# Kernel optimization log

Hardware: AMD Instinct MI355X
Metric: run time of the kernel (lower is better)

## Reference

```python
import jax, jax.numpy as jnp
import numpy as np

T = 16           # number of stochastic-computing cycles (sequential forward calls)
N = 2097152      # parallel stochastic lanes (flattened element count)
BUF_DEP = 4      # shift-register depth (default buf_dep)


def setup_inputs() -> dict:
    key = jax.random.key(0)
    k1, k2 = jax.random.split(key)
    # bitstreams: values in {0,1}, stored as float32 per bstype=torch.float
    dividend = jax.random.randint(k1, (T, N), 0, 2).astype(jnp.float32)
    divisor = jax.random.randint(k2, (T, N), 0, 2).astype(jnp.float32)
    # ShiftReg_init: sr[i] = i % 2, broadcast to input shape -> [BUF_DEP, N]
    sr_init = jnp.tile((jnp.arange(BUF_DEP) % 2).astype(jnp.float32)[:, None], (1, N))
    # 2-bit (log2(buf_dep)) 1-D Sobol sequence scaled to integers 0..3
    rng_table = jnp.array([0, 2, 3, 1], dtype=jnp.int32)
    return {"dividend": dividend, "divisor": divisor, "sr_init": sr_init, "rng_table": rng_table}


def reference(dividend, divisor, sr_init, rng_table):
    T_ = dividend.shape[0]
    buf_dep = sr_init.shape[0]
    # idx starts at 0 and increments each cycle; gather index = rng[idx % buf_dep]
    rng_idx = rng_table[jnp.arange(T_) % buf_dep]  # [T]

    def step(sr, xs):
        dvd, dvs, r = xs
        sel = (dvs == 1).astype(dvd.dtype)                     # divisor_eq_1
        hq = jax.lax.dynamic_index_in_dim(sr, r, axis=0, keepdims=False)  # historic_q [N]
        q = sel * dvd + (1 - sel) * hq                          # quotient [N]
        # ShiftReg push: new value at slot 0, others shift down, oldest dropped
        sr = jnp.concatenate([q[None], sr[:-1]], axis=0)
        return sr, q

    _, quotients = jax.lax.scan(step, sr_init, (dividend, divisor, rng_idx))
    return quotients  # [T, N]
```

## Files before the change

kernel.cpp:

```cpp
#include <hip/hip_runtime.h>


#define SC_T   16
#define SC_BUF 4
#define PHASE  8

typedef float v4f __attribute__((ext_vector_type(4)));

__global__ __launch_bounds__(256) void cordiv_kernel(
    const v4f* __restrict__ dividend,
    const v4f* __restrict__ divisor,
    const v4f* __restrict__ sr_init,
    const int* __restrict__ rng_table,
    v4f*       __restrict__ out,
    int n4)
{
    const int gid = blockIdx.x * blockDim.x + threadIdx.x;
    if (gid >= n4) return;

    const int r0 = rng_table[0];
    const int r1 = rng_table[1];
    const int r2 = rng_table[2];
    const int r3 = rng_table[3];
    const int rtab[SC_BUF] = {r0, r1, r2, r3};

    v4f sr0 = sr_init[0 * n4 + gid];
    v4f sr1 = sr_init[1 * n4 + gid];
    v4f sr2 = sr_init[2 * n4 + gid];
    v4f sr3 = sr_init[3 * n4 + gid];

    v4f dvd[PHASE], dvs[PHASE];

#pragma unroll
    for (int p = 0; p < SC_T / PHASE; ++p) {
        const int tbase = p * PHASE;

#pragma unroll
        for (int i = 0; i < PHASE; ++i) {
            dvd[i] = dividend[(tbase + i) * n4 + gid];
            dvs[i] = divisor [(tbase + i) * n4 + gid];
        }

#pragma unroll
        for (int i = 0; i < PHASE; ++i) {
            const int t = tbase + i;
            const int r = rtab[t & (SC_BUF - 1)];

            const v4f hq = (r == 0) ? sr0 : (r == 1) ? sr1
                         : (r == 2) ? sr2 : sr3;

            v4f q;
            q.x = (dvs[i].x == 1.0f) ? dvd[i].x : hq.x;
            q.y = (dvs[i].y == 1.0f) ? dvd[i].y : hq.y;
            q.z = (dvs[i].z == 1.0f) ? dvd[i].z : hq.z;
            q.w = (dvs[i].w == 1.0f) ? dvd[i].w : hq.w;

            __builtin_nontemporal_store(q, &out[t * n4 + gid]);

            sr3 = sr2; sr2 = sr1; sr1 = sr0; sr0 = q;
        }
    }
}

extern "C" void kernel_launch(void* const* d_in, const int* in_sizes, int n_in,
                              void* d_out, int out_size, void* d_ws, size_t ws_size,
                              hipStream_t stream) {
    const float* dividend = (const float*)d_in[0];
    const float* divisor  = (const float*)d_in[1];
    const float* sr_init  = (const float*)d_in[2];
    const int*   rng      = (const int*)d_in[3];
    float*       out      = (float*)d_out;

    const int n  = in_sizes[0] / SC_T;
    const int n4 = n / 4;

    const int block = 256;
    const int grid  = (n4 + block - 1) / block;

    cordiv_kernel<<<grid, block, 0, stream>>>(
        (const v4f*)dividend, (const v4f*)divisor,
        (const v4f*)sr_init, rng, (v4f*)out, n4);
}
```

Measured before the change: 373.9 us.

## Stage inputs through LDS with direct global-to-LDS loads in chunks of four

Input loads now use global_load_lds, which writes dividend and divisor straight into shared memory in chunks of four time steps instead of holding eight steps in registers. This cuts register pressure, and the intent is better occupancy on a bandwidth-bound stream. The bounds check is gone, so the kernel assumes n4 is a multiple of the block size. Stores switch from nontemporal to regular, and each chunk waits on vmcnt(0), which serialises loads against compute within a chunk.

```diff
diff --git a/kernel.cpp b/kernel.cpp
--- a/kernel.cpp
+++ b/kernel.cpp
@@ -1,13 +1,17 @@
 #include <hip/hip_runtime.h>
+#include <stdint.h>
 
 
 #define SC_T   16
 #define SC_BUF 4
-#define PHASE  8
+#define CHUNK  4
+#define BLOCK  256
 
 typedef float v4f __attribute__((ext_vector_type(4)));
+typedef const __attribute__((address_space(1))) void glb_void;
+typedef __attribute__((address_space(3))) void lds_void;
 
-__global__ __launch_bounds__(256) void cordiv_kernel(
+__global__ __launch_bounds__(BLOCK) void cordiv_kernel(
     const v4f* __restrict__ dividend,
     const v4f* __restrict__ divisor,
     const v4f* __restrict__ sr_init,
@@ -15,8 +19,12 @@
     v4f*       __restrict__ out,
     int n4)
 {
-    const int gid = blockIdx.x * blockDim.x + threadIdx.x;
-    if (gid >= n4) return;
+    __shared__ v4f lds_dvd[CHUNK][BLOCK];
+    __shared__ v4f lds_dvs[CHUNK][BLOCK];
+
+    const int tid   = threadIdx.x;
+    const int gid   = blockIdx.x * BLOCK + tid;
+    const int wbase = tid & ~63;
 
     const int r0 = rng_table[0];
     const int r1 = rng_table[1];
@@ -29,33 +37,39 @@
     v4f sr2 = sr_init[2 * n4 + gid];
     v4f sr3 = sr_init[3 * n4 + gid];
 
-    v4f dvd[PHASE], dvs[PHASE];
+#pragma unroll
+    for (int c = 0; c < SC_T / CHUNK; ++c) {
+#pragma unroll
+        for (int i = 0; i < CHUNK; ++i) {
+            const int t = c * CHUNK + i;
+            __builtin_amdgcn_global_load_lds(
+                (glb_void*)(dividend + (size_t)t * n4 + gid),
+                (lds_void*)&lds_dvd[i][wbase], 16, 0, 0);
+            __builtin_amdgcn_global_load_lds(
+                (glb_void*)(divisor + (size_t)t * n4 + gid),
+                (lds_void*)&lds_dvs[i][wbase], 16, 0, 0);
+        }
+
+        asm volatile("s_waitcnt vmcnt(0)" ::: "memory");
 
 #pragma unroll
-    for (int p = 0; p < SC_T / PHASE; ++p) {
-        const int tbase = p * PHASE;
+        for (int i = 0; i < CHUNK; ++i) {
+            const int t = c * CHUNK + i;
+            const int r = rtab[t & (SC_BUF - 1)];
 
-#pragma unroll
-        for (int i = 0; i < PHASE; ++i) {
-            dvd[i] = dividend[(tbase + i) * n4 + gid];
-            dvs[i] = divisor [(tbase + i) * n4 + gid];
-        }
-
-#pragma unroll
-        for (int i = 0; i < PHASE; ++i) {
-            const int t = tbase + i;
-            const int r = rtab[t & (SC_BUF - 1)];
+            const v4f dvd = lds_dvd[i][tid];
+            const v4f dvs = lds_dvs[i][tid];
 
             const v4f hq = (r == 0) ? sr0 : (r == 1) ? sr1
                          : (r == 2) ? sr2 : sr3;
 
             v4f q;
-            q.x = (dvs[i].x == 1.0f) ? dvd[i].x : hq.x;
-            q.y = (dvs[i].y == 1.0f) ? dvd[i].y : hq.y;
-            q.z = (dvs[i].z == 1.0f) ? dvd[i].z : hq.z;
-            q.w = (dvs[i].w == 1.0f) ? dvd[i].w : hq.w;
+            q.x = (dvs.x == 1.0f) ? dvd.x : hq.x;
+            q.y = (dvs.y == 1.0f) ? dvd.y : hq.y;
+            q.z = (dvs.z == 1.0f) ? dvd.z : hq.z;
+            q.w = (dvs.w == 1.0f) ? dvd.w : hq.w;
 
-            __builtin_nontemporal_store(q, &out[t * n4 + gid]);
+            out[(size_t)t * n4 + gid] = q;
 
             sr3 = sr2; sr2 = sr1; sr1 = sr0; sr0 = q;
         }
@@ -74,10 +88,9 @@
     const int n  = in_sizes[0] / SC_T;
     const int n4 = n / 4;
 
-    const int block = 256;
-    const int grid  = (n4 + block - 1) / block;
+    const int grid = (n4 + BLOCK - 1) / BLOCK;
 
-    cordiv_kernel<<<grid, block, 0, stream>>>(
+    cordiv_kernel<<<grid, BLOCK, 0, stream>>>(
         (const v4f*)dividend, (const v4f*)divisor,
         (const v4f*)sr_init, rng, (v4f*)out, n4);
 }
```

New measurement: 338.9 us. -9.4%, faster.

## Software-pipeline loads with inline asm and two lanes per thread

Applied to the files above, without the earlier changes.

Each thread now handles two vec4 lanes and streams the 16 time steps through a 3-slot register ring. Loads are issued two steps ahead via inline-asm global_load_dwordx4, and the code waits on explicit vmcnt counts, replacing the two batched 8-step load phases. Nontemporal stores become plain stores, and the bounds check is dropped because the grid assumes n4 divides by 512. The aim is steadier memory-level parallelism at lower register cost, but the hand-written vmcnt accounting is fragile and may fight the compiler's own waitcnt insertion.

```diff
diff --git a/kernel.cpp b/kernel.cpp
--- a/kernel.cpp
+++ b/kernel.cpp
@@ -1,11 +1,24 @@
 #include <hip/hip_runtime.h>
+#include <stdint.h>
 
 
-#define SC_T   16
-#define SC_BUF 4
-#define PHASE  8
+#define SC_T    16
+#define D_AHEAD 2
 
 typedef float v4f __attribute__((ext_vector_type(4)));
+
+__device__ __forceinline__ v4f gload(const v4f* __restrict__ p) {
+    v4f r;
+    asm volatile("global_load_dwordx4 %0, %1, off" : "=v"(r) : "v"(p));
+    return r;
+}
+
+#define PIN_WAIT(N, a, b, c, d)                                          \
+    asm volatile("s_waitcnt vmcnt(%c4)"                                  \
+                 : "+v"(a), "+v"(b), "+v"(c), "+v"(d) : "i"(N) : "memory")
+
+#define WAITN(t) (2 * ((t) >= 1) + 2 * ((t) >= 2) + \
+                  4 * ((t) + 1 < SC_T) + 4 * ((t) + 2 < SC_T))
 
 __global__ __launch_bounds__(256) void cordiv_kernel(
     const v4f* __restrict__ dividend,
@@ -15,51 +28,67 @@
     v4f*       __restrict__ out,
     int n4)
 {
-    const int gid = blockIdx.x * blockDim.x + threadIdx.x;
-    if (gid >= n4) return;
+    const int tid = threadIdx.x;
+    const int g0  = blockIdx.x * 512 + tid;
+    const int g1  = g0 + 256;
 
     const int r0 = rng_table[0];
     const int r1 = rng_table[1];
     const int r2 = rng_table[2];
     const int r3 = rng_table[3];
-    const int rtab[SC_BUF] = {r0, r1, r2, r3};
+    const int rtab[4] = {r0, r1, r2, r3};
 
-    v4f sr0 = sr_init[0 * n4 + gid];
-    v4f sr1 = sr_init[1 * n4 + gid];
-    v4f sr2 = sr_init[2 * n4 + gid];
-    v4f sr3 = sr_init[3 * n4 + gid];
+    v4f srA0 = sr_init[0 * n4 + g0], srA1 = sr_init[1 * n4 + g0],
+        srA2 = sr_init[2 * n4 + g0], srA3 = sr_init[3 * n4 + g0];
+    v4f srB0 = sr_init[0 * n4 + g1], srB1 = sr_init[1 * n4 + g1],
+        srB2 = sr_init[2 * n4 + g1], srB3 = sr_init[3 * n4 + g1];
+    asm volatile("" : "+v"(srA0), "+v"(srA1), "+v"(srA2), "+v"(srA3),
+                      "+v"(srB0), "+v"(srB1), "+v"(srB2), "+v"(srB3));
 
-    v4f dvd[PHASE], dvs[PHASE];
+    v4f bD[3][2], bS[3][2];
 
-#pragma unroll
-    for (int p = 0; p < SC_T / PHASE; ++p) {
-        const int tbase = p * PHASE;
+#define ISSUE(t) do {                                                     \
+        const int s_ = (t) % 3;                                           \
+        bD[s_][0] = gload(dividend + (size_t)(t) * n4 + g0);              \
+        bD[s_][1] = gload(dividend + (size_t)(t) * n4 + g1);              \
+        bS[s_][0] = gload(divisor  + (size_t)(t) * n4 + g0);              \
+        bS[s_][1] = gload(divisor  + (size_t)(t) * n4 + g1);              \
+    } while (0)
 
-#pragma unroll
-        for (int i = 0; i < PHASE; ++i) {
-            dvd[i] = dividend[(tbase + i) * n4 + gid];
-            dvs[i] = divisor [(tbase + i) * n4 + gid];
-        }
+#define STEP(t) do {                                                      \
+        if ((t) + D_AHEAD < SC_T) ISSUE((t) + D_AHEAD);                   \
+        const int s_ = (t) % 3;                                           \
+        PIN_WAIT(WAITN(t), bD[s_][0], bD[s_][1], bS[s_][0], bS[s_][1]);   \
+        const int r_ = rtab[(t) & 3];                                     \
+        const v4f hqA = (r_ == 0) ? srA0 : (r_ == 1) ? srA1               \
+                      : (r_ == 2) ? srA2 : srA3;                          \
+        const v4f hqB = (r_ == 0) ? srB0 : (r_ == 1) ? srB1               \
+                      : (r_ == 2) ? srB2 : srB3;                          \
+        v4f qA, qB;                                                       \
+        qA.x = (bS[s_][0].x == 1.0f) ? bD[s_][0].x : hqA.x;               \
+        qA.y = (bS[s_][0].y == 1.0f) ? bD[s_][0].y : hqA.y;               \
+        qA.z = (bS[s_][0].z == 1.0f) ? bD[s_][0].z : hqA.z;               \
+        qA.w = (bS[s_][0].w == 1.0f) ? bD[s_][0].w : hqA.w;               \
+        qB.x = (bS[s_][1].x == 1.0f) ? bD[s_][1].x : hqB.x;               \
+        qB.y = (bS[s_][1].y == 1.0f) ? bD[s_][1].y : hqB.y;               \
+        qB.z = (bS[s_][1].z == 1.0f) ? bD[s_][1].z : hqB.z;               \
+        qB.w = (bS[s_][1].w == 1.0f) ? bD[s_][1].w : hqB.w;               \
+        out[(size_t)(t) * n4 + g0] = qA;                                  \
+        out[(size_t)(t) * n4 + g1] = qB;                                  \
+        srA3 = srA2; srA2 = srA1; srA1 = srA0; srA0 = qA;                 \
+        srB3 = srB2; srB2 = srB1; srB1 = srB0; srB0 = qB;                 \
+    } while (0)
 
-#pragma unroll
-        for (int i = 0; i < PHASE; ++i) {
-            const int t = tbase + i;
-            const int r = rtab[t & (SC_BUF - 1)];
+    ISSUE(0);
+    ISSUE(1);
 
-            const v4f hq = (r == 0) ? sr0 : (r == 1) ? sr1
-                         : (r == 2) ? sr2 : sr3;
+    STEP(0);  STEP(1);  STEP(2);  STEP(3);
+    STEP(4);  STEP(5);  STEP(6);  STEP(7);
+    STEP(8);  STEP(9);  STEP(10); STEP(11);
+    STEP(12); STEP(13); STEP(14); STEP(15);
 
-            v4f q;
-            q.x = (dvs[i].x == 1.0f) ? dvd[i].x : hq.x;
-            q.y = (dvs[i].y == 1.0f) ? dvd[i].y : hq.y;
-            q.z = (dvs[i].z == 1.0f) ? dvd[i].z : hq.z;
-            q.w = (dvs[i].w == 1.0f) ? dvd[i].w : hq.w;
-
-            __builtin_nontemporal_store(q, &out[t * n4 + gid]);
-
-            sr3 = sr2; sr2 = sr1; sr1 = sr0; sr0 = q;
-        }
-    }
+#undef STEP
+#undef ISSUE
 }
 
 extern "C" void kernel_launch(void* const* d_in, const int* in_sizes, int n_in,
@@ -75,7 +104,7 @@
     const int n4 = n / 4;
 
     const int block = 256;
-    const int grid  = (n4 + block - 1) / block;
+    const int grid  = n4 / 512;
 
     cordiv_kernel<<<grid, block, 0, stream>>>(
         (const v4f*)dividend, (const v4f*)divisor,
```

After: 335.8 us. -10.2%, faster.

## Split cordiv into parallel select pass and sequential resolve pass

Applied to the files above, without the earlier changes.

Splits the single fused kernel into two launches. The first is a fully parallel pass over all T*N elements that writes the dividend where the divisor is 1 and a -1 sentinel elsewhere. The second walks the 16 cycles per lane, reading that intermediate back from the output buffer and filling sentinels from the shift register. The aim is more memory-level parallelism in the first pass, but it adds a full extra read and write of the output, drops the nontemporal stores, and adds a second launch. It also relies on grid sizes dividing evenly by 256.

```diff
diff --git a/kernel.cpp b/kernel.cpp
--- a/kernel.cpp
+++ b/kernel.cpp
@@ -1,64 +1,66 @@
 #include <hip/hip_runtime.h>
 
 
-#define SC_T   16
-#define SC_BUF 4
-#define PHASE  8
+#define SC_T 16
 
 typedef float v4f __attribute__((ext_vector_type(4)));
 
-__global__ __launch_bounds__(256) void cordiv_kernel(
-    const v4f* __restrict__ dividend,
-    const v4f* __restrict__ divisor,
+__global__ __launch_bounds__(256) void k_select(
+    const v4f* __restrict__ dvd,
+    const v4f* __restrict__ dvs,
+    v4f*       __restrict__ out,
+    int total4)
+{
+    const int i = blockIdx.x * 256 + threadIdx.x;
+    if (i >= total4) return;
+
+    const v4f a = dvd[i];
+    const v4f s = dvs[i];
+    v4f q;
+    q.x = (s.x == 1.0f) ? a.x : -1.0f;
+    q.y = (s.y == 1.0f) ? a.y : -1.0f;
+    q.z = (s.z == 1.0f) ? a.z : -1.0f;
+    q.w = (s.w == 1.0f) ? a.w : -1.0f;
+    out[i] = q;
+}
+
+__global__ __launch_bounds__(256) void k_resolve(
     const v4f* __restrict__ sr_init,
     const int* __restrict__ rng_table,
     v4f*       __restrict__ out,
     int n4)
 {
-    const int gid = blockIdx.x * blockDim.x + threadIdx.x;
-    if (gid >= n4) return;
+    const int g = blockIdx.x * 256 + threadIdx.x;
+    if (g >= n4) return;
 
     const int r0 = rng_table[0];
     const int r1 = rng_table[1];
     const int r2 = rng_table[2];
     const int r3 = rng_table[3];
-    const int rtab[SC_BUF] = {r0, r1, r2, r3};
+    const int rtab[4] = {r0, r1, r2, r3};
 
-    v4f sr0 = sr_init[0 * n4 + gid];
-    v4f sr1 = sr_init[1 * n4 + gid];
-    v4f sr2 = sr_init[2 * n4 + gid];
-    v4f sr3 = sr_init[3 * n4 + gid];
-
-    v4f dvd[PHASE], dvs[PHASE];
+    v4f sr0 = sr_init[0 * n4 + g];
+    v4f sr1 = sr_init[1 * n4 + g];
+    v4f sr2 = sr_init[2 * n4 + g];
+    v4f sr3 = sr_init[3 * n4 + g];
 
 #pragma unroll
-    for (int p = 0; p < SC_T / PHASE; ++p) {
-        const int tbase = p * PHASE;
+    for (int t = 0; t < SC_T; ++t) {
+        const int r = rtab[t & 3];
+        const v4f v = out[(size_t)t * n4 + g];
 
-#pragma unroll
-        for (int i = 0; i < PHASE; ++i) {
-            dvd[i] = dividend[(tbase + i) * n4 + gid];
-            dvs[i] = divisor [(tbase + i) * n4 + gid];
-        }
+        const v4f hq = (r == 0) ? sr0 : (r == 1) ? sr1
+                     : (r == 2) ? sr2 : sr3;
 
-#pragma unroll
-        for (int i = 0; i < PHASE; ++i) {
-            const int t = tbase + i;
-            const int r = rtab[t & (SC_BUF - 1)];
+        v4f q;
+        q.x = (v.x != -1.0f) ? v.x : hq.x;
+        q.y = (v.y != -1.0f) ? v.y : hq.y;
+        q.z = (v.z != -1.0f) ? v.z : hq.z;
+        q.w = (v.w != -1.0f) ? v.w : hq.w;
 
-            const v4f hq = (r == 0) ? sr0 : (r == 1) ? sr1
-                         : (r == 2) ? sr2 : sr3;
+        out[(size_t)t * n4 + g] = q;
 
-            v4f q;
-            q.x = (dvs[i].x == 1.0f) ? dvd[i].x : hq.x;
-            q.y = (dvs[i].y == 1.0f) ? dvd[i].y : hq.y;
-            q.z = (dvs[i].z == 1.0f) ? dvd[i].z : hq.z;
-            q.w = (dvs[i].w == 1.0f) ? dvd[i].w : hq.w;
-
-            __builtin_nontemporal_store(q, &out[t * n4 + gid]);
-
-            sr3 = sr2; sr2 = sr1; sr1 = sr0; sr0 = q;
-        }
+        sr3 = sr2; sr2 = sr1; sr1 = sr0; sr0 = q;
     }
 }
 
@@ -71,13 +73,13 @@
     const int*   rng      = (const int*)d_in[3];
     float*       out      = (float*)d_out;
 
-    const int n  = in_sizes[0] / SC_T;
-    const int n4 = n / 4;
+    const int total  = in_sizes[0];
+    const int total4 = total / 4;
+    const int n4     = (total / SC_T) / 4;
 
-    const int block = 256;
-    const int grid  = (n4 + block - 1) / block;
+    k_select<<<total4 / 256, 256, 0, stream>>>(
+        (const v4f*)dividend, (const v4f*)divisor, (v4f*)out, total4);
 
-    cordiv_kernel<<<grid, block, 0, stream>>>(
-        (const v4f*)dividend, (const v4f*)divisor,
+    k_resolve<<<n4 / 256, 256, 0, stream>>>(
         (const v4f*)sr_init, rng, (v4f*)out, n4);
 }
```

After: 370.7 us. About the same (-0.8%).
